# Kernel optimization log

Measured on AMD Instinct MI355X. Metric: run time of the kernel, lower is better.

## Reference

```python
import jax, jax.numpy as jnp
import numpy as np

INPUT_SIZE = 21
HIDDEN = 50
OUTPUT = 24
BATCH = 4096
SEQ = 336


def setup_inputs() -> dict:
    key = jax.random.key(0)
    ks = jax.random.split(key, 7)
    s_ih = 1.0 / np.sqrt(HIDDEN)
    x = jax.random.normal(ks[0], (BATCH, SEQ, INPUT_SIZE), dtype=jnp.float32)
    # PyTorch LSTM params: gate order i, f, g, o stacked along dim0
    W_ih = jax.random.uniform(ks[1], (4 * HIDDEN, INPUT_SIZE), minval=-s_ih, maxval=s_ih, dtype=jnp.float32)
    W_hh = jax.random.uniform(ks[2], (4 * HIDDEN, HIDDEN), minval=-s_ih, maxval=s_ih, dtype=jnp.float32)
    b_ih = jax.random.uniform(ks[3], (4 * HIDDEN,), minval=-s_ih, maxval=s_ih, dtype=jnp.float32)
    b_hh = jax.random.uniform(ks[4], (4 * HIDDEN,), minval=-s_ih, maxval=s_ih, dtype=jnp.float32)
    s_fc = 1.0 / np.sqrt(HIDDEN)
    W_fc = jax.random.uniform(ks[5], (OUTPUT, HIDDEN), minval=-s_fc, maxval=s_fc, dtype=jnp.float32)
    b_fc = jax.random.uniform(ks[6], (OUTPUT,), minval=-s_fc, maxval=s_fc, dtype=jnp.float32)
    return {"x": x, "W_ih": W_ih, "W_hh": W_hh, "b_ih": b_ih, "b_hh": b_hh, "W_fc": W_fc, "b_fc": b_fc}


def _lstm_last(x, W_ih, W_hh, b_ih, b_hh):
    B = x.shape[0]
    H = W_hh.shape[1]
    # Precompute input projections for all timesteps: [T, B, 4H]
    x_proj = jnp.einsum('bti,gi->tbg', x, W_ih) + (b_ih + b_hh)

    def step(carry, xp):
        h, c = carry
        gates = xp + h @ W_hh.T  # [B, 4H]
        i_g, f_g, g_g, o_g = jnp.split(gates, 4, axis=-1)
        i_g = jax.nn.sigmoid(i_g)
        f_g = jax.nn.sigmoid(f_g)
        g_g = jnp.tanh(g_g)
        o_g = jax.nn.sigmoid(o_g)
        c = f_g * c + i_g * g_g
        h = o_g * jnp.tanh(c)
        return (h, c), None

    h0 = jnp.zeros((B, H), dtype=x.dtype)
    c0 = jnp.zeros((B, H), dtype=x.dtype)
    (h_last, _), _ = jax.lax.scan(step, (h0, c0), x_proj)
    return h_last


def reference(x, W_ih, W_hh, b_ih, b_hh, W_fc, b_fc):
    h_last = _lstm_last(x, W_ih, W_hh, b_ih, b_hh)  # [B, H]
    return h_last @ W_fc.T + b_fc  # [B, OUTPUT]
```

## Files before the change

### kernel.cpp

```cpp
#include <hip/hip_runtime.h>


#define T_SEQ 336
#define I_IN  21
#define HID   50
#define O_OUT 24
#define MB    16
#define NT    832
#define NTILE 13
#define KB    12

#define AIDX(buf, limb, kb, n, j) (((((buf)*2 + (limb))*KB + (kb))*16 + (n))*8 + (j))

typedef short bf16x8 __attribute__((ext_vector_type(8)));
typedef float f32x4  __attribute__((ext_vector_type(4)));

static __device__ __forceinline__ unsigned short f2bf(float f) {
    unsigned u = __builtin_bit_cast(unsigned, f);
    return (unsigned short)((u + 0x7FFFu + ((u >> 16) & 1u)) >> 16);
}
static __device__ __forceinline__ float bf2f(unsigned short s) {
    unsigned u = ((unsigned)s) << 16;
    return __builtin_bit_cast(float, u);
}
static __device__ __forceinline__ void split2(float v, short& hi, short& lo) {
    const unsigned u = __builtin_bit_cast(unsigned, v);
    hi = (short)(u >> 16);
    const float hf = __builtin_bit_cast(float, u & 0xFFFF0000u);
    const float l  = v - hf;
    lo = (short)(__builtin_bit_cast(unsigned, l) >> 16);
}
static __device__ __forceinline__ float frcp(float v) { return __builtin_amdgcn_rcpf(v); }
static __device__ __forceinline__ float sigm(float v) { return frcp(1.f + __expf(-v)); }
static __device__ __forceinline__ float tanh_f(float v) {
    float av = __builtin_fabsf(v);
    float e  = __expf(-2.f * av);
    float t  = (1.f - e) * frcp(1.f + e);
    return __builtin_copysignf(t, v);
}

__global__ __launch_bounds__(NT)
void lstm_mfma4(const float* __restrict__ x,
                const float* __restrict__ W_ih,
                const float* __restrict__ W_hh,
                const float* __restrict__ b_ih,
                const float* __restrict__ b_hh,
                const float* __restrict__ W_fc,
                const float* __restrict__ b_fc,
                float* __restrict__ out)
{
    __shared__ short sAct[2 * 2 * KB * 16 * 8];

    const int tid  = threadIdx.x;
    const int lane = tid & 63;
    const int wv   = tid >> 6;
    const int nl   = lane & 15;
    const int q    = lane >> 4;
    const int b0   = blockIdx.x * MB;

    for (int i = tid; i < 2 * 2 * KB * 16 * 8; i += NT) sAct[i] = 0;

    bf16x8 Wh[3], Wl[3];
    f32x4  biasv;
    {
        const int p    = wv * 16 + nl;
        const int unit = p >> 2, gate = p & 3;
        const bool vr  = (unit < HID);
        const int orig = gate * HID + unit;
        const int ub   = wv * 4 + q;
        #pragma unroll
        for (int r = 0; r < 4; ++r)
            biasv[r] = (ub < HID) ? (b_ih[r * HID + ub] + b_hh[r * HID + ub]) : 0.f;
        #pragma unroll
        for (int kc = 0; kc < 3; ++kc) {
            #pragma unroll
            for (int j = 0; j < 8; ++j) {
                const int k = kc * 32 + q * 8 + j;
                float w = 0.f;
                if (vr) {
                    if (k < 64) { if (k < HID) w = W_hh[orig * HID + k]; }
                    else { const int ki = k - 64; if (ki < I_IN) w = W_ih[orig * I_IN + ki]; }
                }
                const unsigned short hi = f2bf(w);
                const unsigned short lo = f2bf(w - bf2f(hi));
                Wh[kc][j] = (short)hi;
                Wl[kc][j] = (short)lo;
            }
        }
    }

    __syncthreads();

    const int  sid = tid - (NT - MB * I_IN);
    const bool stg = (sid >= 0);
    const int  sb  = stg ? sid / I_IN : 0;
    const int  sk  = stg ? sid % I_IN : 0;
    const float* xg = x + (size_t)(b0 + sb) * T_SEQ * I_IN + sk;
    if (stg) {
        short hi, lo;
        split2(xg[0], hi, lo);
        sAct[AIDX(0, 0, 8 + (sk >> 3), sb, sk & 7)] = hi;
        sAct[AIDX(0, 1, 8 + (sk >> 3), sb, sk & 7)] = lo;
    }

    const int  uown  = wv * 4 + q;
    const bool uval  = (uown < HID);
    float cst = 0.f;

    for (int t = 0; t < T_SEQ; ++t) {
        const int cur = t & 1, nxt = cur ^ 1;

        float pf = 0.f;
        const bool do_pf = stg && (t + 1 < T_SEQ);
        if (do_pf) pf = xg[(size_t)(t + 1) * I_IN];

        __syncthreads();

        f32x4 aA = biasv;
        f32x4 aB = {0.f, 0.f, 0.f, 0.f};
        #pragma unroll
        for (int kc = 0; kc < 3; ++kc) {
            const int kb = kc * 4 + q;
            const bf16x8 Bh = *(const bf16x8*)&sAct[AIDX(cur, 0, kb, nl, 0)];
            const bf16x8 Bl = *(const bf16x8*)&sAct[AIDX(cur, 1, kb, nl, 0)];
            aA = __builtin_amdgcn_mfma_f32_16x16x32_bf16(Wh[kc], Bh, aA, 0, 0, 0);
            aB = __builtin_amdgcn_mfma_f32_16x16x32_bf16(Wh[kc], Bl, aB, 0, 0, 0);
            aA = __builtin_amdgcn_mfma_f32_16x16x32_bf16(Wl[kc], Bh, aA, 0, 0, 0);
        }

        if (uval) {
            const float gi = aA[0] + aB[0];
            const float gf = aA[1] + aB[1];
            const float gg = aA[2] + aB[2];
            const float go = aA[3] + aB[3];
            float c = cst;
            c = sigm(gf) * c + sigm(gi) * tanh_f(gg);
            cst = c;
            const float h = sigm(go) * tanh_f(c);
            short hi, lo;
            split2(h, hi, lo);
            sAct[AIDX(nxt, 0, uown >> 3, nl, uown & 7)] = hi;
            sAct[AIDX(nxt, 1, uown >> 3, nl, uown & 7)] = lo;
        }

        if (do_pf) {
            short hi, lo;
            split2(pf, hi, lo);
            sAct[AIDX(nxt, 0, 8 + (sk >> 3), sb, sk & 7)] = hi;
            sAct[AIDX(nxt, 1, 8 + (sk >> 3), sb, sk & 7)] = lo;
        }
    }

    __syncthreads();
    if (tid < MB * O_OUT) {
        const int b = tid / O_OUT, o = tid % O_OUT;
        float a = b_fc[o];
        for (int u = 0; u < HID; ++u) {
            const float hv = bf2f((unsigned short)sAct[AIDX(0, 0, u >> 3, b, u & 7)])
                           + bf2f((unsigned short)sAct[AIDX(0, 1, u >> 3, b, u & 7)]);
            a = __builtin_fmaf(hv, W_fc[o * HID + u], a);
        }
        out[(size_t)(b0 + b) * O_OUT + o] = a;
    }
}

extern "C" void kernel_launch(void* const* d_in, const int* in_sizes, int n_in,
                              void* d_out, int out_size, void* d_ws, size_t ws_size,
                              hipStream_t stream)
{
    const float* x    = (const float*)d_in[0];
    const float* W_ih = (const float*)d_in[1];
    const float* W_hh = (const float*)d_in[2];
    const float* b_ih = (const float*)d_in[3];
    const float* b_hh = (const float*)d_in[4];
    const float* W_fc = (const float*)d_in[5];
    const float* b_fc = (const float*)d_in[6];
    float* out = (float*)d_out;

    lstm_mfma4<<<dim3(4096 / MB), dim3(NT), 0, stream>>>(
        x, W_ih, W_hh, b_ih, b_hh, W_fc, b_fc, out);
}
```

Baseline: 372.7 us.

## Give each wave two gate tiles, halving block size, and simplify tanh

Each wavefront now owns two 16-row gate tiles instead of one, so the block shrinks from 13 waves to 7. The shared activations are loaded once per wave and reused across both tiles, and the MFMAs of the two tiles are interleaved to hide latency. The goal is to lower the per-step barrier cost and LDS traffic across the 336-step recurrence. The tanh is rewritten as 1 - 2/(1+exp(2x)), which is cheaper but can overflow exp for large inputs. The x prefetch store also moves before the MFMAs.

```diff
diff --git a/kernel.cpp b/kernel.cpp
--- a/kernel.cpp
+++ b/kernel.cpp
@@ -6,7 +6,7 @@
 #define HID   50
 #define O_OUT 24
 #define MB    16
-#define NT    832
+#define NT    448
 #define NTILE 13
 #define KB    12
 
@@ -33,14 +33,11 @@
 static __device__ __forceinline__ float frcp(float v) { return __builtin_amdgcn_rcpf(v); }
 static __device__ __forceinline__ float sigm(float v) { return frcp(1.f + __expf(-v)); }
 static __device__ __forceinline__ float tanh_f(float v) {
-    float av = __builtin_fabsf(v);
-    float e  = __expf(-2.f * av);
-    float t  = (1.f - e) * frcp(1.f + e);
-    return __builtin_copysignf(t, v);
+    return __builtin_fmaf(-2.f, frcp(1.f + __expf(2.f * v)), 1.f);
 }
 
 __global__ __launch_bounds__(NT)
-void lstm_mfma4(const float* __restrict__ x,
+void lstm_mfma5(const float* __restrict__ x,
                 const float* __restrict__ W_ih,
                 const float* __restrict__ W_hh,
                 const float* __restrict__ b_ih,
@@ -60,17 +57,20 @@
 
     for (int i = tid; i < 2 * 2 * KB * 16 * 8; i += NT) sAct[i] = 0;
 
-    bf16x8 Wh[3], Wl[3];
-    f32x4  biasv;
-    {
-        const int p    = wv * 16 + nl;
+    const bool t1ok = (2 * wv + 1) < NTILE;
+    bf16x8 Wh[2][3], Wl[2][3];
+    f32x4  biasv[2];
+    #pragma unroll
+    for (int tt = 0; tt < 2; ++tt) {
+        const int tile = 2 * wv + tt;
+        const int p    = tile * 16 + nl;
         const int unit = p >> 2, gate = p & 3;
-        const bool vr  = (unit < HID);
+        const bool vr  = (unit < HID) && (tile < NTILE);
         const int orig = gate * HID + unit;
-        const int ub   = wv * 4 + q;
+        const int ub   = tile * 4 + q;
         #pragma unroll
         for (int r = 0; r < 4; ++r)
-            biasv[r] = (ub < HID) ? (b_ih[r * HID + ub] + b_hh[r * HID + ub]) : 0.f;
+            biasv[tt][r] = (ub < HID) ? (b_ih[r * HID + ub] + b_hh[r * HID + ub]) : 0.f;
         #pragma unroll
         for (int kc = 0; kc < 3; ++kc) {
             #pragma unroll
@@ -83,18 +83,17 @@
                 }
                 const unsigned short hi = f2bf(w);
                 const unsigned short lo = f2bf(w - bf2f(hi));
-                Wh[kc][j] = (short)hi;
-                Wl[kc][j] = (short)lo;
+                Wh[tt][kc][j] = (short)hi;
+                Wl[tt][kc][j] = (short)lo;
             }
         }
     }
 
     __syncthreads();
 
-    const int  sid = tid - (NT - MB * I_IN);
-    const bool stg = (sid >= 0);
-    const int  sb  = stg ? sid / I_IN : 0;
-    const int  sk  = stg ? sid % I_IN : 0;
+    const bool stg = tid < MB * I_IN;
+    const int  sb  = stg ? tid / I_IN : 0;
+    const int  sk  = stg ? tid % I_IN : 0;
     const float* xg = x + (size_t)(b0 + sb) * T_SEQ * I_IN + sk;
     if (stg) {
         short hi, lo;
@@ -103,9 +102,9 @@
         sAct[AIDX(0, 1, 8 + (sk >> 3), sb, sk & 7)] = lo;
     }
 
-    const int  uown  = wv * 4 + q;
-    const bool uval  = (uown < HID);
-    float cst = 0.f;
+    const int  uown[2] = {8 * wv + q, 8 * wv + 4 + q};
+    const bool uval[2] = {uown[0] < HID, uown[1] < HID && t1ok};
+    float cst[2] = {0.f, 0.f};
 
     for (int t = 0; t < T_SEQ; ++t) {
         const int cur = t & 1, nxt = cur ^ 1;
@@ -116,31 +115,12 @@
 
         __syncthreads();
 
-        f32x4 aA = biasv;
-        f32x4 aB = {0.f, 0.f, 0.f, 0.f};
+        bf16x8 Bh[3], Bl[3];
         #pragma unroll
         for (int kc = 0; kc < 3; ++kc) {
             const int kb = kc * 4 + q;
-            const bf16x8 Bh = *(const bf16x8*)&sAct[AIDX(cur, 0, kb, nl, 0)];
-            const bf16x8 Bl = *(const bf16x8*)&sAct[AIDX(cur, 1, kb, nl, 0)];
-            aA = __builtin_amdgcn_mfma_f32_16x16x32_bf16(Wh[kc], Bh, aA, 0, 0, 0);
-            aB = __builtin_amdgcn_mfma_f32_16x16x32_bf16(Wh[kc], Bl, aB, 0, 0, 0);
-            aA = __builtin_amdgcn_mfma_f32_16x16x32_bf16(Wl[kc], Bh, aA, 0, 0, 0);
-        }
-
-        if (uval) {
-            const float gi = aA[0] + aB[0];
-            const float gf = aA[1] + aB[1];
-            const float gg = aA[2] + aB[2];
-            const float go = aA[3] + aB[3];
-            float c = cst;
-            c = sigm(gf) * c + sigm(gi) * tanh_f(gg);
-            cst = c;
-            const float h = sigm(go) * tanh_f(c);
-            short hi, lo;
-            split2(h, hi, lo);
-            sAct[AIDX(nxt, 0, uown >> 3, nl, uown & 7)] = hi;
-            sAct[AIDX(nxt, 1, uown >> 3, nl, uown & 7)] = lo;
+            Bh[kc] = *(const bf16x8*)&sAct[AIDX(cur, 0, kb, nl, 0)];
+            Bl[kc] = *(const bf16x8*)&sAct[AIDX(cur, 1, kb, nl, 0)];
         }
 
         if (do_pf) {
@@ -148,6 +128,42 @@
             split2(pf, hi, lo);
             sAct[AIDX(nxt, 0, 8 + (sk >> 3), sb, sk & 7)] = hi;
             sAct[AIDX(nxt, 1, 8 + (sk >> 3), sb, sk & 7)] = lo;
+        }
+
+        f32x4 aA0 = biasv[0], aB0 = {0.f, 0.f, 0.f, 0.f};
+        f32x4 aA1 = biasv[1], aB1 = {0.f, 0.f, 0.f, 0.f};
+        #pragma unroll
+        for (int kc = 0; kc < 3; ++kc) {
+            aA0 = __builtin_amdgcn_mfma_f32_16x16x32_bf16(Wh[0][kc], Bh[kc], aA0, 0, 0, 0);
+            if (t1ok)
+                aA1 = __builtin_amdgcn_mfma_f32_16x16x32_bf16(Wh[1][kc], Bh[kc], aA1, 0, 0, 0);
+            aB0 = __builtin_amdgcn_mfma_f32_16x16x32_bf16(Wh[0][kc], Bl[kc], aB0, 0, 0, 0);
+            if (t1ok)
+                aB1 = __builtin_amdgcn_mfma_f32_16x16x32_bf16(Wh[1][kc], Bl[kc], aB1, 0, 0, 0);
+            aA0 = __builtin_amdgcn_mfma_f32_16x16x32_bf16(Wl[0][kc], Bh[kc], aA0, 0, 0, 0);
+            if (t1ok)
+                aA1 = __builtin_amdgcn_mfma_f32_16x16x32_bf16(Wl[1][kc], Bh[kc], aA1, 0, 0, 0);
+        }
+
+        #pragma unroll
+        for (int tt = 0; tt < 2; ++tt) {
+            if (uval[tt]) {
+                const f32x4& aA = (tt == 0) ? aA0 : aA1;
+                const f32x4& aB = (tt == 0) ? aB0 : aB1;
+                const float gi = aA[0] + aB[0];
+                const float gf = aA[1] + aB[1];
+                const float gg = aA[2] + aB[2];
+                const float go = aA[3] + aB[3];
+                float c = cst[tt];
+                c = __builtin_fmaf(sigm(gf), c, sigm(gi) * tanh_f(gg));
+                cst[tt] = c;
+                const float h = sigm(go) * tanh_f(c);
+                short hi, lo;
+                split2(h, hi, lo);
+                const int u = uown[tt];
+                sAct[AIDX(nxt, 0, u >> 3, nl, u & 7)] = hi;
+                sAct[AIDX(nxt, 1, u >> 3, nl, u & 7)] = lo;
+            }
         }
     }
 
@@ -177,6 +193,6 @@
     const float* b_fc = (const float*)d_in[6];
     float* out = (float*)d_out;
 
-    lstm_mfma4<<<dim3(4096 / MB), dim3(NT), 0, stream>>>(
+    lstm_mfma5<<<dim3(4096 / MB), dim3(NT), 0, stream>>>(
         x, W_ih, W_hh, b_ih, b_hh, W_fc, b_fc, out);
 }
```

After: 432.4 us. 16.0% more time.

## Switch LSTM recurrence from split-bf16 to fp16 activations with split weights

Applied to the files above, without the earlier changes.

Replaces the bf16 hi/lo split of both weights and activations with fp16. Weights are still split into hi/lo parts, but activations (h and x) are stored as a single fp16 value. This cuts the per-step MFMA count from 9 to 6, halves LDS traffic, and removes the split arithmetic on the serial critical path. It also uses a cheaper tanh formula, issues the LDS loads before the x prefetch store, and moves the x staging threads to the first wave group. Activations now keep only fp16 precision, and the new tanh can lose accuracy or overflow for large inputs, which risks accuracy over 336 steps.

```diff
diff --git a/kernel.cpp b/kernel.cpp
--- a/kernel.cpp
+++ b/kernel.cpp
@@ -10,37 +10,19 @@
 #define NTILE 13
 #define KB    12
 
-#define AIDX(buf, limb, kb, n, j) (((((buf)*2 + (limb))*KB + (kb))*16 + (n))*8 + (j))
+#define AIDX(buf, kb, n, j) ((((buf)*KB + (kb))*16 + (n))*8 + (j))
 
-typedef short bf16x8 __attribute__((ext_vector_type(8)));
-typedef float f32x4  __attribute__((ext_vector_type(4)));
+typedef _Float16 f16x8 __attribute__((ext_vector_type(8)));
+typedef float    f32x4 __attribute__((ext_vector_type(4)));
 
-static __device__ __forceinline__ unsigned short f2bf(float f) {
-    unsigned u = __builtin_bit_cast(unsigned, f);
-    return (unsigned short)((u + 0x7FFFu + ((u >> 16) & 1u)) >> 16);
-}
-static __device__ __forceinline__ float bf2f(unsigned short s) {
-    unsigned u = ((unsigned)s) << 16;
-    return __builtin_bit_cast(float, u);
-}
-static __device__ __forceinline__ void split2(float v, short& hi, short& lo) {
-    const unsigned u = __builtin_bit_cast(unsigned, v);
-    hi = (short)(u >> 16);
-    const float hf = __builtin_bit_cast(float, u & 0xFFFF0000u);
-    const float l  = v - hf;
-    lo = (short)(__builtin_bit_cast(unsigned, l) >> 16);
-}
 static __device__ __forceinline__ float frcp(float v) { return __builtin_amdgcn_rcpf(v); }
 static __device__ __forceinline__ float sigm(float v) { return frcp(1.f + __expf(-v)); }
 static __device__ __forceinline__ float tanh_f(float v) {
-    float av = __builtin_fabsf(v);
-    float e  = __expf(-2.f * av);
-    float t  = (1.f - e) * frcp(1.f + e);
-    return __builtin_copysignf(t, v);
+    return __builtin_fmaf(-2.f, frcp(1.f + __expf(2.f * v)), 1.f);
 }
 
 __global__ __launch_bounds__(NT)
-void lstm_mfma4(const float* __restrict__ x,
+void lstm_mfma6(const float* __restrict__ x,
                 const float* __restrict__ W_ih,
                 const float* __restrict__ W_hh,
                 const float* __restrict__ b_ih,
@@ -49,7 +31,7 @@
                 const float* __restrict__ b_fc,
                 float* __restrict__ out)
 {
-    __shared__ short sAct[2 * 2 * KB * 16 * 8];
+    __shared__ _Float16 sAct[2 * KB * 16 * 8];
 
     const int tid  = threadIdx.x;
     const int lane = tid & 63;
@@ -58,10 +40,10 @@
     const int q    = lane >> 4;
     const int b0   = blockIdx.x * MB;
 
-    for (int i = tid; i < 2 * 2 * KB * 16 * 8; i += NT) sAct[i] = 0;
+    for (int i = tid; i < 2 * KB * 16 * 8; i += NT) sAct[i] = (_Float16)0.f;
 
-    bf16x8 Wh[3], Wl[3];
-    f32x4  biasv;
+    f16x8 Wh[3], Wl[3];
+    f32x4 biasv;
     {
         const int p    = wv * 16 + nl;
         const int unit = p >> 2, gate = p & 3;
@@ -81,31 +63,31 @@
                     if (k < 64) { if (k < HID) w = W_hh[orig * HID + k]; }
                     else { const int ki = k - 64; if (ki < I_IN) w = W_ih[orig * I_IN + ki]; }
                 }
-                const unsigned short hi = f2bf(w);
-                const unsigned short lo = f2bf(w - bf2f(hi));
-                Wh[kc][j] = (short)hi;
-                Wl[kc][j] = (short)lo;
+                const _Float16 hi = (_Float16)w;
+                const _Float16 lo = (_Float16)(w - (float)hi);
+                Wh[kc][j] = hi;
+                Wl[kc][j] = lo;
             }
         }
     }
 
     __syncthreads();
 
-    const int  sid = tid - (NT - MB * I_IN);
-    const bool stg = (sid >= 0);
-    const int  sb  = stg ? sid / I_IN : 0;
-    const int  sk  = stg ? sid % I_IN : 0;
+    const bool stg = tid < MB * I_IN;
+    const int  sb  = stg ? tid / I_IN : 0;
+    const int  sk  = stg ? tid % I_IN : 0;
     const float* xg = x + (size_t)(b0 + sb) * T_SEQ * I_IN + sk;
-    if (stg) {
-        short hi, lo;
-        split2(xg[0], hi, lo);
-        sAct[AIDX(0, 0, 8 + (sk >> 3), sb, sk & 7)] = hi;
-        sAct[AIDX(0, 1, 8 + (sk >> 3), sb, sk & 7)] = lo;
-    }
+    const int  xoff = AIDX(0, 8 + (sk >> 3), sb, sk & 7);
+    if (stg) sAct[xoff] = (_Float16)xg[0];
 
-    const int  uown  = wv * 4 + q;
-    const bool uval  = (uown < HID);
+    const int  uown = wv * 4 + q;
+    const bool uval = (uown < HID);
+    const int  hoff = AIDX(0, uown >> 3, nl, uown & 7);
     float cst = 0.f;
+
+    const _Float16* bbase0 = &sAct[AIDX(0, q, nl, 0)];
+    const _Float16* bbase1 = &sAct[AIDX(1, q, nl, 0)];
+    const int BUFS = KB * 16 * 8;
 
     for (int t = 0; t < T_SEQ; ++t) {
         const int cur = t & 1, nxt = cur ^ 1;
@@ -116,17 +98,21 @@
 
         __syncthreads();
 
+        const _Float16* bb = cur ? bbase1 : bbase0;
+        f16x8 B0 = *(const f16x8*)(bb);
+        f16x8 B1 = *(const f16x8*)(bb + 4 * 16 * 8);
+        f16x8 B2 = *(const f16x8*)(bb + 8 * 16 * 8);
+
+        if (do_pf) sAct[nxt * BUFS + xoff] = (_Float16)pf;
+
         f32x4 aA = biasv;
         f32x4 aB = {0.f, 0.f, 0.f, 0.f};
-        #pragma unroll
-        for (int kc = 0; kc < 3; ++kc) {
-            const int kb = kc * 4 + q;
-            const bf16x8 Bh = *(const bf16x8*)&sAct[AIDX(cur, 0, kb, nl, 0)];
-            const bf16x8 Bl = *(const bf16x8*)&sAct[AIDX(cur, 1, kb, nl, 0)];
-            aA = __builtin_amdgcn_mfma_f32_16x16x32_bf16(Wh[kc], Bh, aA, 0, 0, 0);
-            aB = __builtin_amdgcn_mfma_f32_16x16x32_bf16(Wh[kc], Bl, aB, 0, 0, 0);
-            aA = __builtin_amdgcn_mfma_f32_16x16x32_bf16(Wl[kc], Bh, aA, 0, 0, 0);
-        }
+        aA = __builtin_amdgcn_mfma_f32_16x16x32_f16(Wh[0], B0, aA, 0, 0, 0);
+        aB = __builtin_amdgcn_mfma_f32_16x16x32_f16(Wl[0], B0, aB, 0, 0, 0);
+        aA = __builtin_amdgcn_mfma_f32_16x16x32_f16(Wh[1], B1, aA, 0, 0, 0);
+        aB = __builtin_amdgcn_mfma_f32_16x16x32_f16(Wl[1], B1, aB, 0, 0, 0);
+        aA = __builtin_amdgcn_mfma_f32_16x16x32_f16(Wh[2], B2, aA, 0, 0, 0);
+        aB = __builtin_amdgcn_mfma_f32_16x16x32_f16(Wl[2], B2, aB, 0, 0, 0);
 
         if (uval) {
             const float gi = aA[0] + aB[0];
@@ -134,20 +120,10 @@
             const float gg = aA[2] + aB[2];
             const float go = aA[3] + aB[3];
             float c = cst;
-            c = sigm(gf) * c + sigm(gi) * tanh_f(gg);
+            c = __builtin_fmaf(sigm(gf), c, sigm(gi) * tanh_f(gg));
             cst = c;
             const float h = sigm(go) * tanh_f(c);
-            short hi, lo;
-            split2(h, hi, lo);
-            sAct[AIDX(nxt, 0, uown >> 3, nl, uown & 7)] = hi;
-            sAct[AIDX(nxt, 1, uown >> 3, nl, uown & 7)] = lo;
-        }
-
-        if (do_pf) {
-            short hi, lo;
-            split2(pf, hi, lo);
-            sAct[AIDX(nxt, 0, 8 + (sk >> 3), sb, sk & 7)] = hi;
-            sAct[AIDX(nxt, 1, 8 + (sk >> 3), sb, sk & 7)] = lo;
+            sAct[nxt * BUFS + hoff] = (_Float16)h;
         }
     }
 
@@ -156,8 +132,7 @@
         const int b = tid / O_OUT, o = tid % O_OUT;
         float a = b_fc[o];
         for (int u = 0; u < HID; ++u) {
-            const float hv = bf2f((unsigned short)sAct[AIDX(0, 0, u >> 3, b, u & 7)])
-                           + bf2f((unsigned short)sAct[AIDX(0, 1, u >> 3, b, u & 7)]);
+            const float hv = (float)sAct[AIDX(0, u >> 3, b, u & 7)];
             a = __builtin_fmaf(hv, W_fc[o * HID + u], a);
         }
         out[(size_t)(b0 + b) * O_OUT + o] = a;
@@ -177,6 +152,6 @@
     const float* b_fc = (const float*)d_in[6];
     float* out = (float*)d_out;
 
-    lstm_mfma4<<<dim3(4096 / MB), dim3(NT), 0, stream>>>(
+    lstm_mfma6<<<dim3(4096 / MB), dim3(NT), 0, stream>>>(
         x, W_ih, W_hh, b_ih, b_hh, W_fc, b_fc, out);
 }
```

Result: slower. 408.9 us (+9.7%).
